# Optimization experiments

Hardware: AMD Instinct MI355X
Metric: run time of the kernel (lower is better)

## Reference

```python
import jax, jax.numpy as jnp
import numpy as np


def euler2mat(omega):
    # omega: [3] Euler angles (x, y, z); R = Rz @ Ry @ Rx
    sx, sy, sz = jnp.sin(omega[0]), jnp.sin(omega[1]), jnp.sin(omega[2])
    cx, cy, cz = jnp.cos(omega[0]), jnp.cos(omega[1]), jnp.cos(omega[2])
    Rx = jnp.array([[1.0, 0.0, 0.0], [0.0, cx, -sx], [0.0, sx, cx]], dtype=omega.dtype)
    Ry = jnp.array([[cy, 0.0, sy], [0.0, 1.0, 0.0], [-sy, 0.0, cy]], dtype=omega.dtype)
    Rz = jnp.array([[cz, -sz, 0.0], [sz, cz, 0.0], [0.0, 0.0, 1.0]], dtype=omega.dtype)
    return Rz @ Ry @ Rx


def cd_loss(pred, gt):
    # pred: [N,3], gt: [K,3] -> mean over N of min_k ||pred_n - gt_k||^2
    a = jnp.sum(pred * pred, axis=1)[:, None]          # [N,1]
    b = jnp.sum(gt * gt, axis=1)[None, :]              # [1,K]
    c = jnp.einsum('ik,jk->ij', pred, gt)              # [N,K]
    dist = a + b - 2.0 * c                             # [N,K]
    return jnp.mean(jnp.min(dist, axis=1))


def setup_inputs() -> dict:
    key = jax.random.key(0)
    k1, k2, k3, k4 = jax.random.split(key, 4)
    return {
        "visual_points": jax.random.normal(k1, (16384, 3), dtype=jnp.float32),
        "tactile_points": jax.random.normal(k2, (2048, 3), dtype=jnp.float32),
        "model_points": jax.random.normal(k3, (8192, 3), dtype=jnp.float32),
        "scale": jnp.ones((), dtype=jnp.float32),
        "state": jax.random.normal(k4, (6,), dtype=jnp.float32),
    }


def reference(visual_points, tactile_points, model_points, scale, state):
    t = state[0:3]                 # translation [3]
    r = euler2mat(state[3:6])      # rotation [3,3]
    vc = ((visual_points - t[None, :]) @ r) / scale
    tc = ((tactile_points - t[None, :]) @ r) / scale
    E = 1.0 * cd_loss(vc, model_points) + 0.1 * cd_loss(tc, model_points)
    return E
```

## Files before the change

kernel.cpp:

```cpp
#include <hip/hip_runtime.h>
#include <hip/hip_bf16.h>

#define NVIS   16384
#define NTAC   2048
#define NPRED  (NVIS + NTAC)
#define NMODEL 8192

#define BLK    256
#define PPT    3
#define TILE   (BLK * PPT)
#define NTILE  (NPRED / TILE)
#define CHUNK  128
#define NCHUNK (NMODEL / CHUNK)

#define BIGF   3.4e38f


__global__ __launch_bounds__(BLK) void cd_partial_kernel(
    const float* __restrict__ vis,
    const float* __restrict__ tac,
    const float* __restrict__ model,
    const float* __restrict__ scale,
    const float* __restrict__ state,
    unsigned* __restrict__ pmin)
{
    __shared__ float4 sm[CHUNK];

    const int tid   = threadIdx.x;
    const int tile  = blockIdx.x;
    const int chunk = blockIdx.y;

    if (tid < CHUNK) {
        const float ax = state[3], ay = state[4], az = state[5];
        const float sx = sinf(ax), cx = cosf(ax);
        const float sy = sinf(ay), cy = cosf(ay);
        const float sz = sinf(az), cz = cosf(az);
        const float R00 = cz * cy;
        const float R01 = cz * sy * sx - sz * cx;
        const float R02 = cz * sy * cx + sz * sx;
        const float R10 = sz * cy;
        const float R11 = sz * sy * sx + cz * cx;
        const float R12 = sz * sy * cx - cz * sx;
        const float R20 = -sy;
        const float R21 = cy * sx;
        const float R22 = cy * cx;
        const float t0 = state[0], t1 = state[1], t2 = state[2];
        const float s  = scale[0];

        const float* mp = model + 3 * (chunk * CHUNK + tid);
        const float mx = mp[0], my = mp[1], mz = mp[2];
        const float wx = fmaf(s, mx * R00 + my * R01 + mz * R02, t0);
        const float wy = fmaf(s, mx * R10 + my * R11 + mz * R12, t1);
        const float wz = fmaf(s, mx * R20 + my * R21 + mz * R22, t2);
        sm[tid] = make_float4(wx, wy, wz, 0.5f * (wx * wx + wy * wy + wz * wz));
    }

    float nx[PPT], ny[PPT], nz[PPT], pa[PPT];
    #pragma unroll
    for (int k = 0; k < PPT; ++k) {
        const int pid = tile * TILE + k * BLK + tid;
        const float* pp = (pid < NVIS) ? (vis + 3 * pid) : (tac + 3 * (pid - NVIS));
        const float p0 = pp[0], p1 = pp[1], p2 = pp[2];
        pa[k] = p0 * p0 + p1 * p1 + p2 * p2;
        nx[k] = -p0; ny[k] = -p1; nz[k] = -p2;
    }

    __syncthreads();

    float bA[PPT], bB[PPT];
    #pragma unroll
    for (int k = 0; k < PPT; ++k) { bA[k] = BIGF; bB[k] = BIGF; }

    #pragma unroll 8
    for (int j = 0; j < CHUNK; j += 2) {
        const float4 mA = sm[j];
        const float4 mB = sm[j + 1];
        #pragma unroll
        for (int k = 0; k < PPT; ++k) {
            bA[k] = fminf(bA[k], fmaf(nx[k], mA.x, fmaf(ny[k], mA.y, fmaf(nz[k], mA.z, mA.w))));
            bB[k] = fminf(bB[k], fmaf(nx[k], mB.x, fmaf(ny[k], mB.y, fmaf(nz[k], mB.z, mB.w))));
        }
    }

    const int pbase = tile * TILE + tid;
    #pragma unroll
    for (int k = 0; k < PPT; ++k) {
        const float b = fminf(bA[k], bB[k]);
        atomicMin(&pmin[pbase + k * BLK], __float_as_uint(fmaf(2.0f, b, pa[k])));
    }
}

__global__ __launch_bounds__(1024) void cd_reduce_kernel(
    const unsigned* __restrict__ pmin,
    const float* __restrict__ scale,
    float* __restrict__ out)
{
    const int tid = threadIdx.x;

    float vs = 0.0f, ts = 0.0f;
    #pragma unroll
    for (int it = 0; it < NPRED / 1024; ++it) {
        const int pid = it * 1024 + tid;
        const float v = __uint_as_float(pmin[pid]);
        if (pid < NVIS) vs += v; else ts += v;
    }

    #pragma unroll
    for (int off = 32; off > 0; off >>= 1) {
        vs += __shfl_down(vs, off, 64);
        ts += __shfl_down(ts, off, 64);
    }

    __shared__ float svis[16], stac[16];
    if ((tid & 63) == 0) { svis[tid >> 6] = vs; stac[tid >> 6] = ts; }
    __syncthreads();

    if (tid == 0) {
        float v = 0.0f, t = 0.0f;
        #pragma unroll
        for (int w = 0; w < 16; ++w) { v += svis[w]; t += stac[w]; }
        const float s = scale[0];
        const float inv2 = 1.0f / (s * s);
        out[0] = inv2 * (v * (1.0f / (float)NVIS) + t * (0.1f / (float)NTAC));
    }
}

extern "C" void kernel_launch(void* const* d_in, const int* in_sizes, int n_in,
                              void* d_out, int out_size, void* d_ws, size_t ws_size,
                              hipStream_t stream) {
    const float* vis   = (const float*)d_in[0];
    const float* tac   = (const float*)d_in[1];
    const float* model = (const float*)d_in[2];
    const float* scale = (const float*)d_in[3];
    const float* state = (const float*)d_in[4];
    float* out = (float*)d_out;

    unsigned* pmin = (unsigned*)d_ws;

    hipMemsetAsync(pmin, 0xFF, NPRED * sizeof(unsigned), stream);

    dim3 grid(NTILE, NCHUNK);
    cd_partial_kernel<<<grid, BLK, 0, stream>>>(vis, tac, model, scale, state, pmin);

    cd_reduce_kernel<<<1, 1024, 0, stream>>>(pmin, scale, out);
}
```

Measured before the change: 76.27 us.

## Assign points per wavefront, loop over all model points, fuse final reduction

```diff
diff --git a/kernel.cpp b/kernel.cpp
--- a/kernel.cpp
+++ b/kernel.cpp
@@ -7,121 +7,140 @@
 #define NMODEL 8192
 
 #define BLK    256
-#define PPT    3
-#define TILE   (BLK * PPT)
-#define NTILE  (NPRED / TILE)
-#define CHUNK  128
-#define NCHUNK (NMODEL / CHUNK)
+#define PPW    6
+#define PPB    24
+#define NBLK   (NPRED / PPB)
+#define MCHUNK 512
+#define NMC    (NMODEL / MCHUNK)
 
 #define BIGF   3.4e38f
+#define W_VIS  (1.0f / 16384.0f)
+#define W_TAC  (0.1f / 2048.0f)
 
 
-__global__ __launch_bounds__(BLK) void cd_partial_kernel(
-    const float* __restrict__ vis,
-    const float* __restrict__ tac,
+__global__ __launch_bounds__(BLK) void cd_init_kernel(
     const float* __restrict__ model,
     const float* __restrict__ scale,
     const float* __restrict__ state,
-    unsigned* __restrict__ pmin)
+    float4* __restrict__ model4,
+    int* __restrict__ counter)
 {
-    __shared__ float4 sm[CHUNK];
+    const int tid = threadIdx.x;
+    if (blockIdx.x == 0 && tid == 0)
+        __hip_atomic_store(counter, 0, __ATOMIC_RELEASE, __HIP_MEMORY_SCOPE_AGENT);
 
-    const int tid   = threadIdx.x;
-    const int tile  = blockIdx.x;
-    const int chunk = blockIdx.y;
+    const float ax = state[3], ay = state[4], az = state[5];
+    const float sx = sinf(ax), cx = cosf(ax);
+    const float sy = sinf(ay), cy = cosf(ay);
+    const float sz = sinf(az), cz = cosf(az);
+    const float R00 = cz * cy;
+    const float R01 = cz * sy * sx - sz * cx;
+    const float R02 = cz * sy * cx + sz * sx;
+    const float R10 = sz * cy;
+    const float R11 = sz * sy * sx + cz * cx;
+    const float R12 = sz * sy * cx - cz * sx;
+    const float R20 = -sy;
+    const float R21 = cy * sx;
+    const float R22 = cy * cx;
+    const float t0 = state[0], t1 = state[1], t2 = state[2];
+    const float s  = scale[0];
 
-    if (tid < CHUNK) {
-        const float ax = state[3], ay = state[4], az = state[5];
-        const float sx = sinf(ax), cx = cosf(ax);
-        const float sy = sinf(ay), cy = cosf(ay);
-        const float sz = sinf(az), cz = cosf(az);
-        const float R00 = cz * cy;
-        const float R01 = cz * sy * sx - sz * cx;
-        const float R02 = cz * sy * cx + sz * sx;
-        const float R10 = sz * cy;
-        const float R11 = sz * sy * sx + cz * cx;
-        const float R12 = sz * sy * cx - cz * sx;
-        const float R20 = -sy;
-        const float R21 = cy * sx;
-        const float R22 = cy * cx;
-        const float t0 = state[0], t1 = state[1], t2 = state[2];
-        const float s  = scale[0];
+    const int mid = blockIdx.x * BLK + tid;
+    const float* mp = model + 3 * mid;
+    const float mx = mp[0], my = mp[1], mz = mp[2];
+    const float wx = fmaf(s, mx * R00 + my * R01 + mz * R02, t0);
+    const float wy = fmaf(s, mx * R10 + my * R11 + mz * R12, t1);
+    const float wz = fmaf(s, mx * R20 + my * R21 + mz * R22, t2);
+    model4[mid] = make_float4(wx, wy, wz, 0.5f * (wx * wx + wy * wy + wz * wz));
+}
 
-        const float* mp = model + 3 * (chunk * CHUNK + tid);
-        const float mx = mp[0], my = mp[1], mz = mp[2];
-        const float wx = fmaf(s, mx * R00 + my * R01 + mz * R02, t0);
-        const float wy = fmaf(s, mx * R10 + my * R11 + mz * R12, t1);
-        const float wz = fmaf(s, mx * R20 + my * R21 + mz * R22, t2);
-        sm[tid] = make_float4(wx, wy, wz, 0.5f * (wx * wx + wy * wy + wz * wz));
+__global__ __launch_bounds__(BLK) void cd_main_kernel(
+    const float* __restrict__ vis,
+    const float* __restrict__ tac,
+    const float4* __restrict__ model4,
+    const float* __restrict__ scale,
+    float* __restrict__ bsum,
+    int* __restrict__ counter,
+    float* __restrict__ out)
+{
+    __shared__ float4 sm[MCHUNK];
+    __shared__ float wsums[4];
+    __shared__ int lastflag;
+
+    const int tid  = threadIdx.x;
+    const int bid  = blockIdx.x;
+    const int lane = tid & 63;
+    const int wid  = tid >> 6;
+    const int base = bid * PPB + wid * PPW;
+
+    float nx[PPW], ny[PPW], nz[PPW], pa[PPW], bmin[PPW];
+    #pragma unroll
+    for (int q = 0; q < PPW; ++q) {
+        const int pid = base + q;
+        const float* pp = (pid < NVIS) ? (vis + 3 * pid) : (tac + 3 * (pid - NVIS));
+        const float p0 = pp[0], p1 = pp[1], p2 = pp[2];
+        pa[q] = p0 * p0 + p1 * p1 + p2 * p2;
+        nx[q] = -p0; ny[q] = -p1; nz[q] = -p2;
+        bmin[q] = BIGF;
     }
 
-    float nx[PPT], ny[PPT], nz[PPT], pa[PPT];
-    #pragma unroll
-    for (int k = 0; k < PPT; ++k) {
-        const int pid = tile * TILE + k * BLK + tid;
-        const float* pp = (pid < NVIS) ? (vis + 3 * pid) : (tac + 3 * (pid - NVIS));
-        const float p0 = pp[0], p1 = pp[1], p2 = pp[2];
-        pa[k] = p0 * p0 + p1 * p1 + p2 * p2;
-        nx[k] = -p0; ny[k] = -p1; nz[k] = -p2;
-    }
+    for (int c = 0; c < NMC; ++c) {
+        __syncthreads();
+        sm[tid]       = model4[c * MCHUNK + tid];
+        sm[tid + BLK] = model4[c * MCHUNK + BLK + tid];
+        __syncthreads();
 
-    __syncthreads();
-
-    float bA[PPT], bB[PPT];
-    #pragma unroll
-    for (int k = 0; k < PPT; ++k) { bA[k] = BIGF; bB[k] = BIGF; }
-
-    #pragma unroll 8
-    for (int j = 0; j < CHUNK; j += 2) {
-        const float4 mA = sm[j];
-        const float4 mB = sm[j + 1];
         #pragma unroll
-        for (int k = 0; k < PPT; ++k) {
-            bA[k] = fminf(bA[k], fmaf(nx[k], mA.x, fmaf(ny[k], mA.y, fmaf(nz[k], mA.z, mA.w))));
-            bB[k] = fminf(bB[k], fmaf(nx[k], mB.x, fmaf(ny[k], mB.y, fmaf(nz[k], mB.z, mB.w))));
+        for (int i = 0; i < MCHUNK / 64; ++i) {
+            const float4 m = sm[i * 64 + lane];
+            #pragma unroll
+            for (int q = 0; q < PPW; ++q)
+                bmin[q] = fminf(bmin[q],
+                    fmaf(nx[q], m.x, fmaf(ny[q], m.y, fmaf(nz[q], m.z, m.w))));
         }
     }
 
-    const int pbase = tile * TILE + tid;
     #pragma unroll
-    for (int k = 0; k < PPT; ++k) {
-        const float b = fminf(bA[k], bB[k]);
-        atomicMin(&pmin[pbase + k * BLK], __float_as_uint(fmaf(2.0f, b, pa[k])));
-    }
-}
-
-__global__ __launch_bounds__(1024) void cd_reduce_kernel(
-    const unsigned* __restrict__ pmin,
-    const float* __restrict__ scale,
-    float* __restrict__ out)
-{
-    const int tid = threadIdx.x;
-
-    float vs = 0.0f, ts = 0.0f;
-    #pragma unroll
-    for (int it = 0; it < NPRED / 1024; ++it) {
-        const int pid = it * 1024 + tid;
-        const float v = __uint_as_float(pmin[pid]);
-        if (pid < NVIS) vs += v; else ts += v;
+    for (int q = 0; q < PPW; ++q) {
+        #pragma unroll
+        for (int off = 32; off > 0; off >>= 1)
+            bmin[q] = fminf(bmin[q], __shfl_xor(bmin[q], off, 64));
     }
 
+    float wsum = 0.0f;
     #pragma unroll
-    for (int off = 32; off > 0; off >>= 1) {
-        vs += __shfl_down(vs, off, 64);
-        ts += __shfl_down(ts, off, 64);
+    for (int q = 0; q < PPW; ++q) {
+        const int pid = base + q;
+        const float w = (pid < NVIS) ? W_VIS : W_TAC;
+        wsum = fmaf(w, fmaf(2.0f, bmin[q], pa[q]), wsum);
     }
 
-    __shared__ float svis[16], stac[16];
-    if ((tid & 63) == 0) { svis[tid >> 6] = vs; stac[tid >> 6] = ts; }
+    if (lane == 0) wsums[wid] = wsum;
     __syncthreads();
 
     if (tid == 0) {
-        float v = 0.0f, t = 0.0f;
+        const float s = wsums[0] + wsums[1] + wsums[2] + wsums[3];
+        __hip_atomic_store(&bsum[bid], s, __ATOMIC_RELEASE, __HIP_MEMORY_SCOPE_AGENT);
+        const int old = __hip_atomic_fetch_add(counter, 1, __ATOMIC_ACQ_REL,
+                                               __HIP_MEMORY_SCOPE_AGENT);
+        lastflag = (old == NBLK - 1);
+    }
+    __syncthreads();
+
+    if (lastflag) {
+        float s = 0.0f;
+        for (int i = tid; i < NBLK; i += BLK)
+            s += __hip_atomic_load(&bsum[i], __ATOMIC_RELAXED, __HIP_MEMORY_SCOPE_AGENT);
         #pragma unroll
-        for (int w = 0; w < 16; ++w) { v += svis[w]; t += stac[w]; }
-        const float s = scale[0];
-        const float inv2 = 1.0f / (s * s);
-        out[0] = inv2 * (v * (1.0f / (float)NVIS) + t * (0.1f / (float)NTAC));
+        for (int off = 32; off > 0; off >>= 1)
+            s += __shfl_xor(s, off, 64);
+        __syncthreads();
+        if (lane == 0) wsums[wid] = s;
+        __syncthreads();
+        if (tid == 0) {
+            const float sc = scale[0];
+            out[0] = (wsums[0] + wsums[1] + wsums[2] + wsums[3]) / (sc * sc);
+        }
     }
 }
 
@@ -135,12 +154,12 @@
     const float* state = (const float*)d_in[4];
     float* out = (float*)d_out;
 
-    unsigned* pmin = (unsigned*)d_ws;
+    float4* model4  = (float4*)d_ws;
+    float*  bsum    = (float*)(model4 + NMODEL);
+    int*    counter = (int*)(bsum + NBLK);
 
-    hipMemsetAsync(pmin, 0xFF, NPRED * sizeof(unsigned), stream);
-
-    dim3 grid(NTILE, NCHUNK);
-    cd_partial_kernel<<<grid, BLK, 0, stream>>>(vis, tac, model, scale, state, pmin);
-
-    cd_reduce_kernel<<<1, 1024, 0, stream>>>(pmin, scale, out);
+    cd_init_kernel<<<NMODEL / BLK, BLK, 0, stream>>>(model, scale, state,
+                                                     model4, counter);
+    cd_main_kernel<<<NBLK, BLK, 0, stream>>>(vis, tac, model4, scale,
+                                             bsum, counter, out);
 }
```

New measurement: 104.2 us. +36.7%, slower.
